# Kernel optimization log

Measured on AMD Instinct MI355X. Metric: run time of the kernel, lower is better.

Reference implementation:

```python
import jax, jax.numpy as jnp
import numpy as np

HEADS = 8
HID = 128
N_A = 10000
N_B = 10000
E = 120000
NG = 8  # graphs in batch
F_A = 256
F_B = 128
NEG_SLOPE = 0.2


def _gat(h_src, h_dst, src, dst, ws, wd, a_s, a_d, bias, num_dst):
    """PyG GATConv, bipartite, concat=False, add_self_loops=False."""
    hs = (h_src @ ws).reshape(-1, HEADS, HID)   # [N_src, H, C]
    hd = (h_dst @ wd).reshape(-1, HEADS, HID)   # [N_dst, H, C]
    al_s = jnp.sum(hs * a_s, axis=-1)           # [N_src, H]
    al_d = jnp.sum(hd * a_d, axis=-1)           # [N_dst, H]
    e = jax.nn.leaky_relu(al_s[src] + al_d[dst], NEG_SLOPE)  # [E, H]
    m = jax.ops.segment_max(e, dst, num_segments=num_dst)
    ex = jnp.exp(e - m[dst])
    denom = jax.ops.segment_sum(ex, dst, num_segments=num_dst)
    alpha = ex / (denom[dst] + 1e-16)           # segment softmax over in-edges
    msg = hs[src] * alpha[:, :, None]           # [E, H, C]
    out = jax.ops.segment_sum(msg, dst, num_segments=num_dst)
    return out.mean(axis=1) + bias              # concat=False -> head mean + bias


def _mean_pool(x, batch, num_graphs):
    s = jax.ops.segment_sum(x, batch, num_segments=num_graphs)
    cnt = jax.ops.segment_sum(jnp.ones((x.shape[0],), x.dtype), batch, num_segments=num_graphs)
    return s / jnp.maximum(cnt, 1.0)[:, None]


def setup_inputs() -> dict:
    key = jax.random.key(0)
    ks = iter(jax.random.split(key, 48))
    rn = lambda shape, s=0.05: jax.random.normal(next(ks), shape, jnp.float32) * s
    inp = {
        'x_a': jax.random.normal(next(ks), (N_A, F_A), jnp.float32),
        'x_b': jax.random.normal(next(ks), (N_B, F_B), jnp.float32),
        'edge_ab': jax.random.randint(next(ks), (2, E), 0, N_A, jnp.int32),
        'edge_ba': jax.random.randint(next(ks), (2, E), 0, N_B, jnp.int32),
        'batch_a': jnp.sort(jax.random.randint(next(ks), (N_A,), 0, NG, jnp.int32)),
        'batch_b': jnp.sort(jax.random.randint(next(ks), (N_B,), 0, NG, jnp.int32)),
        'lin_a_w': rn((F_A, HID)), 'lin_a_b': rn((HID,)),
        'lin_b_w': rn((F_B, HID)), 'lin_b_b': rn((HID,)),
        'fc_w': rn((2 * HID, 1)), 'fc_b': rn((1,)),
    }
    for layer in ('1', '2'):
        for rel in ('ab', 'ba'):
            inp[f'w{layer}s_{rel}'] = rn((HID, HEADS * HID))
            inp[f'w{layer}d_{rel}'] = rn((HID, HEADS * HID))
            inp[f'a{layer}s_{rel}'] = rn((HEADS, HID))
            inp[f'a{layer}d_{rel}'] = rn((HEADS, HID))
            inp[f'b{layer}_{rel}'] = rn((HID,))
    return inp


def reference(x_a, x_b, edge_ab, edge_ba, batch_a, batch_b,
              lin_a_w, lin_a_b, lin_b_w, lin_b_b, fc_w, fc_b,
              w1s_ab, w1d_ab, a1s_ab, a1d_ab, b1_ab,
              w1s_ba, w1d_ba, a1s_ba, a1d_ba, b1_ba,
              w2s_ab, w2d_ab, a2s_ab, a2d_ab, b2_ab,
              w2s_ba, w2d_ba, a2s_ba, a2d_ba, b2_ba):
    ha = jax.nn.relu(x_a @ lin_a_w + lin_a_b)
    hb = jax.nn.relu(x_b @ lin_b_w + lin_b_b)
    # layer 1 (each dst type receives exactly one relation -> HeteroConv mean is identity)
    hb1 = _gat(ha, hb, edge_ab[0], edge_ab[1], w1s_ab, w1d_ab, a1s_ab, a1d_ab, b1_ab, N_B)
    ha1 = _gat(hb, ha, edge_ba[0], edge_ba[1], w1s_ba, w1d_ba, a1s_ba, a1d_ba, b1_ba, N_A)
    ha1 = jax.nn.relu(ha1)
    hb1 = jax.nn.relu(hb1)
    # layer 2
    hb2 = _gat(ha1, hb1, edge_ab[0], edge_ab[1], w2s_ab, w2d_ab, a2s_ab, a2d_ab, b2_ab, N_B)
    ha2 = _gat(hb1, ha1, edge_ba[0], edge_ba[1], w2s_ba, w2d_ba, a2s_ba, a2d_ba, b2_ba, N_A)
    pa = _mean_pool(ha2, batch_a, NG)
    pb = _mean_pool(hb2, batch_b, NG)
    g = jnp.concatenate([pa, pb], axis=1)       # [NG, 2*HID]
    return (g @ fc_w + fc_b).squeeze(-1)        # [NG]
```

## Files before the change

kernel.cpp:

```cpp
#include <hip/hip_runtime.h>
#include <math.h>

#define HID 128
#define HEADS 8

typedef __attribute__((ext_vector_type(8))) short s16x8;
typedef __attribute__((ext_vector_type(4))) float f32x4;

__device__ __forceinline__ unsigned short bf16_rne(float x) {
  unsigned u = __float_as_uint(x);
  unsigned r = u + 0x7FFFu + ((u >> 16) & 1u);
  return (unsigned short)(r >> 16);
}
__device__ __forceinline__ float bf16f(unsigned short h) {
  return __uint_as_float(((unsigned)h) << 16);
}

struct PrepArgs {
  const float* W[8];
  const float* a[8];
  unsigned short* WThi[4];
  unsigned short* WTlo[4];
  float* v[8];
};
struct PrepX {
  const float* lwa; const float* lwb;
  unsigned short *wa_hi, *wa_lo, *wb_hi, *wb_lo;
  int KA, KB, nwa, nwb;
};

__global__ __launch_bounds__(256) void prep_hist(
    PrepArgs p, PrepX px,
    const int* __restrict__ dst_ab, const int* __restrict__ dst_ba,
    int* __restrict__ cnt_ab, int* __restrict__ cnt_ba, int E)
{
  int bid = blockIdx.x;
  if (bid < 2048) {
    int g = bid >> 9;
    int idx = ((bid & 511) << 8) + threadIdx.x;
    int kidx = idx & 1023;
    int c = idx >> 10;
    int h = kidx >> 7, k = kidx & 127;
    float wv = p.W[2 * g][(size_t)k * (HEADS * HID) + h * HID + c];
    unsigned short hi = bf16_rne(wv);
    unsigned short lo = bf16_rne(wv - bf16f(hi));
    p.WThi[g][idx] = hi;
    p.WTlo[g][idx] = lo;
  } else if (bid < 2080) {
    int u = bid - 2048;
    int wi = u >> 2;
    int gid = ((u & 3) << 8) + threadIdx.x;
    int k = gid >> 3, h = gid & 7;
    const float* wr = p.W[wi] + (size_t)k * (HEADS * HID) + h * HID;
    const float* ar = p.a[wi] + (size_t)h * HID;
    float s = 0.f;
    for (int c = 0; c < HID; c++) s = fmaf(wr[c], ar[c], s);
    p.v[wi][gid] = s;
  } else if (bid < 2080 + px.nwa) {
    int idx = (bid - 2080) * 256 + threadIdx.x;
    if (idx < px.KA * HID) {
      int k = idx % px.KA, c = idx / px.KA;
      float wv = px.lwa[(size_t)k * HID + c];
      unsigned short hi = bf16_rne(wv);
      unsigned short lo = bf16_rne(wv - bf16f(hi));
      px.wa_hi[idx] = hi;
      px.wa_lo[idx] = lo;
    }
  } else if (bid < 2080 + px.nwa + px.nwb) {
    int idx = (bid - 2080 - px.nwa) * 256 + threadIdx.x;
    if (idx < px.KB * HID) {
      int k = idx % px.KB, c = idx / px.KB;
      float wv = px.lwb[(size_t)k * HID + c];
      unsigned short hi = bf16_rne(wv);
      unsigned short lo = bf16_rne(wv - bf16f(hi));
      px.wb_hi[idx] = hi;
      px.wb_lo[idx] = lo;
    }
  } else {
    int gid = (bid - 2080 - px.nwa - px.nwb) * 256 + threadIdx.x;
    if (gid < E) atomicAdd(&cnt_ab[dst_ab[gid]], 1);
    else if (gid < 2 * E) atomicAdd(&cnt_ba[dst_ba[gid - E]], 1);
  }
}

__global__ __launch_bounds__(1024) void scan2(
    const int* __restrict__ cnt_ab, const int* __restrict__ cnt_ba,
    int* __restrict__ ip_ab, int* __restrict__ ip_ba, int n_ab, int n_ba)
{
  const int* cnt = (blockIdx.x == 0) ? cnt_ab : cnt_ba;
  int* indptr = (blockIdx.x == 0) ? ip_ab : ip_ba;
  int n = (blockIdx.x == 0) ? n_ab : n_ba;
  __shared__ int parts[1024];
  const int tid = threadIdx.x;
  const int base = tid * 10;
  int local[10];
  int s = 0;
#pragma unroll
  for (int j = 0; j < 10; j++) {
    int v = (base + j < n) ? cnt[base + j] : 0;
    local[j] = v; s += v;
  }
  parts[tid] = s;
  __syncthreads();
  for (int off = 1; off < 1024; off <<= 1) {
    int v = (tid >= off) ? parts[tid - off] : 0;
    __syncthreads();
    parts[tid] += v;
    __syncthreads();
  }
  int ex = parts[tid] - s;
#pragma unroll
  for (int j = 0; j < 10; j++) {
    if (base + j < n) indptr[base + j] = ex;
    ex += local[j];
  }
  if (tid == 1023) indptr[n] = parts[1023];
}

__global__ __launch_bounds__(256) void scatter2(
    const int* __restrict__ edge_ab, const int* __restrict__ edge_ba,
    const int* __restrict__ ip_ab, const int* __restrict__ ip_ba,
    int* __restrict__ cur_ab, int* __restrict__ cur_ba,
    int* __restrict__ srcs_ab, int* __restrict__ srcs_ba, int E)
{
  int gid = blockIdx.x * 256 + threadIdx.x;
  if (gid < E) {
    int d = edge_ab[E + gid];
    int pos = ip_ab[d] + atomicAdd(&cur_ab[d], 1);
    srcs_ab[pos] = edge_ab[gid];
  } else if (gid < 2 * E) {
    int g = gid - E;
    int d = edge_ba[E + g];
    int pos = ip_ba[d] + atomicAdd(&cur_ba[d], 1);
    srcs_ba[pos] = edge_ba[g];
  }
}

struct ISeg {
  const float* A;
  const unsigned short* Bhi; const unsigned short* Blo;
  float* out; const float* bias; int M; int K; int yb;
};

__global__ __launch_bounds__(256) void gemm_mfma_in(ISeg s0, ISeg s1)
{
  __shared__ __align__(16) unsigned short smem[12288];
  const int tid = threadIdx.x;
  const float* A; const unsigned short *Bhi, *Blo; const float* bias; float* out;
  int M, K, ytile;
  if ((int)blockIdx.x < s0.yb) {
    A = s0.A; Bhi = s0.Bhi; Blo = s0.Blo; out = s0.out; bias = s0.bias;
    M = s0.M; K = s0.K; ytile = blockIdx.x;
  } else {
    A = s1.A; Bhi = s1.Bhi; Blo = s1.Blo; out = s1.out; bias = s1.bias;
    M = s1.M; K = s1.K; ytile = blockIdx.x - s0.yb;
  }
  const int bm = ytile * 64;
  const int nks = K >> 5;

  const int sr = tid >> 2;
  const int sg = tid & 3;
  const int g1 = sg ^ ((sr >> 1) & 3);
  const int sr2 = sr + 64;
  const int g2 = sg ^ ((sr2 >> 1) & 3);
  const int aslot  = sr * 32 + g1 * 8;
  const int bslotA = sr * 32 + g1 * 8;
  const int bslotB = sr2 * 32 + g2 * 8;
  const int gr = bm + sr;
  const bool arow_ok = (gr < M);
  const float* gA = A + (size_t)gr * K + sg * 8;
  const unsigned short* gB0 = Bhi + (size_t)sr  * K + sg * 8;
  const unsigned short* gB1 = Bhi + (size_t)sr2 * K + sg * 8;
  const unsigned short* gC0 = Blo + (size_t)sr  * K + sg * 8;
  const unsigned short* gC1 = Blo + (size_t)sr2 * K + sg * 8;

  const int l = tid & 63;
  const int w = tid >> 6;
  const int kg = l >> 4;
  int aoff[4], boff[2];
#pragma unroll
  for (int mi = 0; mi < 4; mi++) {
    int r = mi * 16 + (l & 15);
    aoff[mi] = r * 32 + (kg ^ ((r >> 1) & 3)) * 8;
  }
#pragma unroll
  for (int ni = 0; ni < 2; ni++) {
    int r = w * 32 + ni * 16 + (l & 15);
    boff[ni] = r * 32 + (kg ^ ((r >> 1) & 3)) * 8;
  }

  f32x4 acc[4][2];
  const f32x4 z4 = {0.f, 0.f, 0.f, 0.f};
#pragma unroll
  for (int mi = 0; mi < 4; mi++)
#pragma unroll
    for (int ni = 0; ni < 2; ni++) acc[mi][ni] = z4;

  float4 fa0 = make_float4(0.f, 0.f, 0.f, 0.f), fa1 = fa0;
  if (arow_ok) { fa0 = *(const float4*)gA; fa1 = *(const float4*)(gA + 4); }
  uint4 rB0 = *(const uint4*)gB0;
  uint4 rB1 = *(const uint4*)gB1;
  uint4 rC0 = *(const uint4*)gC0;
  uint4 rC1 = *(const uint4*)gC1;

  for (int ks = 0; ks < nks; ks++) {
    {
      const float f[8] = {fa0.x, fa0.y, fa0.z, fa0.w, fa1.x, fa1.y, fa1.z, fa1.w};
      unsigned au[4], lu[4];
#pragma unroll
      for (int i = 0; i < 4; i++) {
        unsigned short h0 = bf16_rne(f[2 * i]);
        unsigned short l0 = bf16_rne(f[2 * i] - bf16f(h0));
        unsigned short h1 = bf16_rne(f[2 * i + 1]);
        unsigned short l1 = bf16_rne(f[2 * i + 1] - bf16f(h1));
        au[i] = (unsigned)h0 | ((unsigned)h1 << 16);
        lu[i] = (unsigned)l0 | ((unsigned)l1 << 16);
      }
      *(uint4*)&smem[aslot]        = make_uint4(au[0], au[1], au[2], au[3]);
      *(uint4*)&smem[2048 + aslot] = make_uint4(lu[0], lu[1], lu[2], lu[3]);
    }
    *(uint4*)&smem[4096 + bslotA] = rB0;
    *(uint4*)&smem[4096 + bslotB] = rB1;
    *(uint4*)&smem[8192 + bslotA] = rC0;
    *(uint4*)&smem[8192 + bslotB] = rC1;
    __syncthreads();
    if (ks < nks - 1) {
      const int k0 = (ks + 1) * 32;
      if (arow_ok) {
        fa0 = *(const float4*)(gA + k0);
        fa1 = *(const float4*)(gA + k0 + 4);
      }
      rB0 = *(const uint4*)(gB0 + k0);
// ... 176 lines not shown
    if (s >= 0) {
      float v = als[(size_t)s * HEADS + h] + aldn;
      v = v > 0.f ? v : 0.2f * v;
      ex = expf(v);
    }
    int elim = deg - e0; if (elim > 8) elim = 8;
    for (int e8 = 0; e8 < elim; e8++) {
      int ss = __shfl(s, e8 * 8);
      const float2 hvt = *(const float2*)(hsrc + (size_t)ss * HID + 2 * lane);
#pragma unroll
      for (int hh = 0; hh < 8; hh++) {
        float a = __shfl(ex, e8 * 8 + hh);
        acc[2 * hh]     = fmaf(a, hvt.x, acc[2 * hh]);
        acc[2 * hh + 1] = fmaf(a, hvt.y, acc[2 * hh + 1]);
      }
    }
  }
#pragma unroll
  for (int hh = 0; hh < 8; hh++) {
    float dh = __shfl(den, hh);
    float inv = 1.f / (dh + 1e-16f);
    float x0 = acc[2 * hh] * inv;
    float x1 = acc[2 * hh + 1] * inv;
    unsigned short h0 = bf16_rne(x0), h1 = bf16_rne(x1);
    unsigned short l0 = bf16_rne(x0 - bf16f(h0)), l1 = bf16_rne(x1 - bf16f(h1));
    *(unsigned*)(zh + hh * HID + 2 * lane) = (unsigned)h0 | ((unsigned)h1 << 16);
    *(unsigned*)(zl + hh * HID + 2 * lane) = (unsigned)l0 | ((unsigned)l1 << 16);
  }
}

struct MSeg {
  const unsigned short* Ahi; const unsigned short* Alo;
  const unsigned short* Bhi; const unsigned short* Blo;
  int M; int yb;
};

__global__ __launch_bounds__(256, 2) void gemm_mfma_splitk(
    MSeg s0, MSeg s1, float* __restrict__ P, int Mtot, int KS)
{
  __shared__ __align__(16) unsigned short smem[12288];
  const int tid = threadIdx.x;
  const unsigned short *Ahi, *Alo, *Bhi, *Blo; int M, ytile, rowbase;
  if ((int)blockIdx.x < s0.yb) {
    Ahi = s0.Ahi; Alo = s0.Alo; Bhi = s0.Bhi; Blo = s0.Blo;
    M = s0.M; ytile = blockIdx.x; rowbase = 0;
  } else {
    Ahi = s1.Ahi; Alo = s1.Alo; Bhi = s1.Bhi; Blo = s1.Blo;
    M = s1.M; ytile = blockIdx.x - s0.yb; rowbase = s0.yb * 64;
  }
  const int bm = ytile * 64;
  const int kchunk = 1024 / KS;
  const int kbeg = blockIdx.y * kchunk;
  const int nks = kchunk / 32;

  const int sr = tid >> 2;
  const int sg = tid & 3;
  const int g1 = sg ^ ((sr >> 1) & 3);
  const int sr2 = sr + 64;
  const int g2 = sg ^ ((sr2 >> 1) & 3);
  const int aslot  = sr * 32 + g1 * 8;
  const int bslotA = sr * 32 + g1 * 8;
  const int bslotB = sr2 * 32 + g2 * 8;
  const unsigned short* gA  = Ahi + (size_t)(bm + sr) * 1024 + kbeg + sg * 8;
  const unsigned short* gAl = Alo + (size_t)(bm + sr) * 1024 + kbeg + sg * 8;
  const unsigned short* gB0 = Bhi + (size_t)sr  * 1024 + kbeg + sg * 8;
  const unsigned short* gB1 = Bhi + (size_t)sr2 * 1024 + kbeg + sg * 8;
  const unsigned short* gC0 = Blo + (size_t)sr  * 1024 + kbeg + sg * 8;
  const unsigned short* gC1 = Blo + (size_t)sr2 * 1024 + kbeg + sg * 8;

  const int l = tid & 63;
  const int w = tid >> 6;
  const int kg = l >> 4;
  int aoff[4], boff[2];
#pragma unroll
  for (int mi = 0; mi < 4; mi++) {
    int r = mi * 16 + (l & 15);
    aoff[mi] = r * 32 + (kg ^ ((r >> 1) & 3)) * 8;
  }
#pragma unroll
  for (int ni = 0; ni < 2; ni++) {
    int r = w * 32 + ni * 16 + (l & 15);
    boff[ni] = r * 32 + (kg ^ ((r >> 1) & 3)) * 8;
  }

  f32x4 acc[4][2];
  const f32x4 z4 = {0.f, 0.f, 0.f, 0.f};
#pragma unroll
  for (int mi = 0; mi < 4; mi++)
#pragma unroll
    for (int ni = 0; ni < 2; ni++) acc[mi][ni] = z4;

  uint4 rA  = *(const uint4*)gA;
  uint4 rAl = *(const uint4*)gAl;
  uint4 rB0 = *(const uint4*)gB0;
  uint4 rB1 = *(const uint4*)gB1;
  uint4 rC0 = *(const uint4*)gC0;
  uint4 rC1 = *(const uint4*)gC1;

  for (int ks = 0; ks < nks; ks++) {
    *(uint4*)&smem[aslot]         = rA;
    *(uint4*)&smem[2048 + aslot]  = rAl;
    *(uint4*)&smem[4096 + bslotA] = rB0;
    *(uint4*)&smem[4096 + bslotB] = rB1;
    *(uint4*)&smem[8192 + bslotA] = rC0;
    *(uint4*)&smem[8192 + bslotB] = rC1;
    __syncthreads();
    if (ks < nks - 1) {
      const int k0 = (ks + 1) * 32;
      rA  = *(const uint4*)(gA  + k0);
      rAl = *(const uint4*)(gAl + k0);
      rB0 = *(const uint4*)(gB0 + k0);
      rB1 = *(const uint4*)(gB1 + k0);
      rC0 = *(const uint4*)(gC0 + k0);
      rC1 = *(const uint4*)(gC1 + k0);
    }
    s16x8 bh0 = *(const s16x8*)&smem[4096 + boff[0]];
    s16x8 bh1 = *(const s16x8*)&smem[4096 + boff[1]];
    s16x8 bl0 = *(const s16x8*)&smem[8192 + boff[0]];
    s16x8 bl1 = *(const s16x8*)&smem[8192 + boff[1]];
#pragma unroll
    for (int mi = 0; mi < 4; mi++) {
      s16x8 ah = *(const s16x8*)&smem[aoff[mi]];
      s16x8 al = *(const s16x8*)&smem[2048 + aoff[mi]];
      acc[mi][0] = __builtin_amdgcn_mfma_f32_16x16x32_bf16(ah, bh0, acc[mi][0], 0, 0, 0);
      acc[mi][1] = __builtin_amdgcn_mfma_f32_16x16x32_bf16(ah, bh1, acc[mi][1], 0, 0, 0);
      acc[mi][0] = __builtin_amdgcn_mfma_f32_16x16x32_bf16(ah, bl0, acc[mi][0], 0, 0, 0);
      acc[mi][1] = __builtin_amdgcn_mfma_f32_16x16x32_bf16(ah, bl1, acc[mi][1], 0, 0, 0);
      acc[mi][0] = __builtin_amdgcn_mfma_f32_16x16x32_bf16(al, bh0, acc[mi][0], 0, 0, 0);
      acc[mi][1] = __builtin_amdgcn_mfma_f32_16x16x32_bf16(al, bh1, acc[mi][1], 0, 0, 0);
      acc[mi][0] = __builtin_amdgcn_mfma_f32_16x16x32_bf16(al, bl0, acc[mi][0], 0, 0, 0);
      acc[mi][1] = __builtin_amdgcn_mfma_f32_16x16x32_bf16(al, bl1, acc[mi][1], 0, 0, 0);
    }
    __syncthreads();
  }

  const int q = l >> 4, cl = l & 15;
  const size_t prow0 = (size_t)blockIdx.y * Mtot + rowbase + bm;
#pragma unroll
  for (int ni = 0; ni < 2; ni++) {
    const int col = w * 32 + ni * 16 + cl;
#pragma unroll
    for (int mi = 0; mi < 4; mi++) {
      const int r0 = mi * 16 + q * 4;
      const f32x4 v = acc[mi][ni];
#pragma unroll
      for (int j = 0; j < 4; j++) {
        const int r = r0 + j;
        if (bm + r < M) P[(prow0 + r) * HID + col] = v[j];
      }
    }
  }
}

struct RSeg { float* out; const float* bias; int M; int rowbase; };

__global__ __launch_bounds__(256) void reduce_epi(
    const float* __restrict__ P, int Mtot, int KS, float scale, int do_relu,
    RSeg s0, RSeg s1)
{
  int idx = blockIdx.x * 256 + threadIdx.x;
  if (idx >= Mtot * 32) return;
  int r = idx >> 5;
  int c = (idx & 31) << 2;
  float* outp; const float* bias; int rl;
  if (s1.M > 0 && r >= s1.rowbase) {
    rl = r - s1.rowbase; if (rl >= s1.M) return; outp = s1.out; bias = s1.bias;
  } else {
    rl = r; if (rl >= s0.M) return; outp = s0.out; bias = s0.bias;
  }
  float4 acc = make_float4(0.f, 0.f, 0.f, 0.f);
  for (int z = 0; z < KS; z++) {
    const float4 v = *(const float4*)(P + ((size_t)z * Mtot + r) * HID + c);
    acc.x += v.x; acc.y += v.y; acc.z += v.z; acc.w += v.w;
  }
  const float4 b = *(const float4*)(bias + c);
  acc.x = acc.x * scale + b.x;
  acc.y = acc.y * scale + b.y;
  acc.z = acc.z * scale + b.z;
  acc.w = acc.w * scale + b.w;
  if (do_relu) {
    acc.x = acc.x > 0.f ? acc.x : 0.f;
    acc.y = acc.y > 0.f ? acc.y : 0.f;
    acc.z = acc.z > 0.f ? acc.z : 0.f;
    acc.w = acc.w > 0.f ? acc.w : 0.f;
  }
  *(float4*)(outp + (size_t)rl * HID + c) = acc;
}

__global__ __launch_bounds__(256) void pool_fin(
    const float* __restrict__ ha, const float* __restrict__ hb,
    const int* __restrict__ batch_a, const int* __restrict__ batch_b,
    const float* __restrict__ fc_w, const float* __restrict__ fc_b,
    float* __restrict__ gsum, int* __restrict__ ticket,
    float* __restrict__ out, int na, int nb, int ng)
{
  const bool isA = blockIdx.x < 160;
  const float* h = isA ? ha : hb;
  const int* batch = isA ? batch_a : batch_b;
  const float* wseg = isA ? fc_w : fc_w + HID;
  float* gs = isA ? gsum : gsum + 8;
  const int n = isA ? na : nb;
  const int b = isA ? blockIdx.x : blockIdx.x - 160;

  __shared__ float sg[8];
  __shared__ int lastf;
  if (threadIdx.x < 8) sg[threadIdx.x] = 0.f;
  __syncthreads();
  const int lane = threadIdx.x & 63;
  const int wv = threadIdx.x >> 6;
  const int gw = b * 4 + wv;
  const int tw = 160 * 4;
  const float2 w2 = *(const float2*)(wseg + lane * 2);
  for (int r = gw; r < n; r += tw) {
    float2 hv = *(const float2*)(h + (size_t)r * HID + lane * 2);
    float s = hv.x * w2.x + hv.y * w2.y;
#pragma unroll
    for (int off = 32; off > 0; off >>= 1) s += __shfl_down(s, off, 64);
    if (lane == 0) atomicAdd(&sg[batch[r]], s);
  }
  __syncthreads();
  if (threadIdx.x < 8) atomicAdd(&gs[threadIdx.x], sg[threadIdx.x]);
  if (threadIdx.x == 0) {
    __threadfence();
    int tk = atomicAdd(ticket, 1);
    lastf = (tk == (int)gridDim.x - 1);
  }
  __syncthreads();
  if (lastf) {
    int g = threadIdx.x;
    if (g < ng) {
      int l, r, lo;
      l = 0; r = na; while (l < r) { int m = (l + r) >> 1; if (batch_a[m] < g) l = m + 1; else r = m; } lo = l;
      r = na; while (l < r) { int m = (l + r) >> 1; if (batch_a[m] < g + 1) l = m + 1; else r = m; }
      int ca = l - lo; if (ca < 1) ca = 1;
      l = 0; r = nb; while (l < r) { int m = (l + r) >> 1; if (batch_b[m] < g) l = m + 1; else r = m; } lo = l;
      r = nb; while (l < r) { int m = (l + r) >> 1; if (batch_b[m] < g + 1) l = m + 1; else r = m; }
      int cb = l - lo; if (cb < 1) cb = 1;
      float va = atomicAdd(&gsum[g], 0.f);
      float vb = atomicAdd(&gsum[8 + g], 0.f);
      out[g] = va / (float)ca + vb / (float)cb + fc_b[0];
    }
  }
}

extern "C" void kernel_launch(void* const* d_in, const int* in_sizes, int n_in,
                              void* d_out, int out_size, void* d_ws, size_t ws_size,
                              hipStream_t stream)
{
  const float* x_a = (const float*)d_in[0];
  const float* x_b = (const float*)d_in[1];
  const int* edge_ab = (const int*)d_in[2];
  const int* edge_ba = (const int*)d_in[3];
  const int* batch_a = (const int*)d_in[4];
  const int* batch_b = (const int*)d_in[5];
  const float* lin_a_w = (const float*)d_in[6];
  const float* lin_a_b = (const float*)d_in[7];
  const float* lin_b_w = (const float*)d_in[8];
  const float* lin_b_b = (const float*)d_in[9];
  const float* fc_w = (const float*)d_in[10];
  const float* fc_b = (const float*)d_in[11];

  const int NA = in_sizes[4];
  const int NB = in_sizes[5];
  const int E  = in_sizes[2] / 2;
  const int FA = in_sizes[0] / NA;
  const int FB = in_sizes[1] / NB;
  const int NG = out_size;
  const int NMAX = NA > NB ? NA : NB;
  const int NAp = (NA + 127) & ~127, NBp = (NB + 127) & ~127;
  const int NMAXp = NAp > NBp ? NAp : NBp;
  const int Mtot = NAp + NBp;

  auto al256 = [](size_t b) { return (b + 255) & ~(size_t)255; };
  size_t fixed = 0;
  fixed += 3 * al256((size_t)NAp * HID * 4) + 3 * al256((size_t)NBp * HID * 4);
  fixed += 2 * al256((size_t)NMAXp * 1024 * 2);
  fixed += al256((size_t)8 * 131072 * 2);
  fixed += 2 * al256((size_t)FA * HID * 2) + 2 * al256((size_t)FB * HID * 2);
  fixed += al256((size_t)8 * HID * HEADS * 4);
  fixed += 2 * al256((size_t)NAp * HEADS * 4) + 2 * al256((size_t)NBp * HEADS * 4);
  fixed += al256(((size_t)4 * NMAX + 24) * 4);
  fixed += al256((size_t)(NB + 1) * 4) + al256((size_t)(NA + 1) * 4);
  fixed += 2 * al256((size_t)E * 4);
  fixed += 8192;
  const size_t zba_sz = 2 * al256((size_t)NAp * 1024 * 2);
  const size_t pslice = al256((size_t)Mtot * HID * 4);

  int KS = 4; bool dual = true;
  if (fixed + zba_sz + 4 * pslice <= ws_size)      { dual = true;  KS = 4; }
  else if (fixed + zba_sz + 2 * pslice <= ws_size) { dual = true;  KS = 2; }
  else if (fixed + 4 * pslice <= ws_size)          { dual = false; KS = 4; }
  else if (fixed + 2 * pslice <= ws_size)          { dual = false; KS = 2; }
  else if (fixed + 1 * pslice <= ws_size)          { dual = false; KS = 1; }
  else return;

  char* w = (char*)d_ws;
  auto carve = [&](size_t bytes) -> void* {
    void* p = (void*)w;
    w += (bytes + 255) & ~(size_t)255;
    return p;
  };
  float* ha0 = (float*)carve((size_t)NAp * HID * 4);
  float* hb0 = (float*)carve((size_t)NBp * HID * 4);
  float* ha1 = (float*)carve((size_t)NAp * HID * 4);
  float* hb1 = (float*)carve((size_t)NBp * HID * 4);
  float* ha2 = (float*)carve((size_t)NAp * HID * 4);
  float* hb2 = (float*)carve((size_t)NBp * HID * 4);
  unsigned short* zab_hi = (unsigned short*)carve((size_t)NMAXp * 1024 * 2);
  unsigned short* zab_lo = (unsigned short*)carve((size_t)NMAXp * 1024 * 2);
  unsigned short* zba_hi = dual ? (unsigned short*)carve((size_t)NAp * 1024 * 2) : zab_hi;
  unsigned short* zba_lo = dual ? (unsigned short*)carve((size_t)NAp * 1024 * 2) : zab_lo;
  float* P = (float*)carve((size_t)KS * Mtot * HID * 4);
  unsigned short* WT = (unsigned short*)carve((size_t)8 * 131072 * 2);
  unsigned short* wa_hi = (unsigned short*)carve((size_t)FA * HID * 2);
  unsigned short* wa_lo = (unsigned short*)carve((size_t)FA * HID * 2);
  unsigned short* wb_hi = (unsigned short*)carve((size_t)FB * HID * 2);
  unsigned short* wb_lo = (unsigned short*)carve((size_t)FB * HID * 2);
  float* vv  = (float*)carve((size_t)8 * HID * HEADS * 4);
  float* als_ab = (float*)carve((size_t)NAp * HEADS * 4);
  float* ald_ab = (float*)carve((size_t)NBp * HEADS * 4);
  float* als_ba = (float*)carve((size_t)NBp * HEADS * 4);
  float* ald_ba = (float*)carve((size_t)NAp * HEADS * 4);
  int* csrblk = (int*)carve(((size_t)4 * NMAX + 24) * 4);
  int* indptr_ab = (int*)carve((size_t)(NB + 1) * 4);
  int* indptr_ba = (int*)carve((size_t)(NA + 1) * 4);
  int* srcs_ab   = (int*)carve((size_t)E * 4);
  int* srcs_ba   = (int*)carve((size_t)E * 4);
  if ((size_t)(w - (char*)d_ws) > ws_size) return;

  int* cnt_ab = csrblk;
  int* cnt_ba = csrblk + NMAX;
  int* cur_ab = csrblk + 2 * NMAX;
  int* cur_ba = csrblk + 3 * NMAX;
  float* gsum = (float*)(csrblk + 4 * NMAX);
  int* ticket = csrblk + 4 * NMAX + 16;

  hipMemsetAsync(csrblk, 0, ((size_t)4 * NMAX + 24) * 4, stream);

  PrepArgs pa;
  const int wi_idx[8] = {12, 13, 17, 18, 22, 23, 27, 28};
  const int ai_idx[8] = {14, 15, 19, 20, 24, 25, 29, 30};
  for (int i = 0; i < 8; i++) {
    pa.W[i] = (const float*)d_in[wi_idx[i]];
    pa.a[i] = (const float*)d_in[ai_idx[i]];
    pa.v[i] = vv + (size_t)i * HID * HEADS;
  }
  for (int g = 0; g < 4; g++) {
    pa.WThi[g] = WT + (size_t)g * 131072;
    pa.WTlo[g] = WT + (size_t)(4 + g) * 131072;
  }
  PrepX px;
  px.lwa = lin_a_w; px.lwb = lin_b_w;
  px.wa_hi = wa_hi; px.wa_lo = wa_lo; px.wb_hi = wb_hi; px.wb_lo = wb_lo;
  px.KA = FA; px.KB = FB;
  px.nwa = (FA * HID + 255) / 256;
  px.nwb = (FB * HID + 255) / 256;
  const int hist_b = (2 * E + 255) / 256;
  prep_hist<<<2080 + px.nwa + px.nwb + hist_b, 256, 0, stream>>>(
      pa, px, edge_ab + E, edge_ba + E, cnt_ab, cnt_ba, E);
  scan2<<<2, 1024, 0, stream>>>(cnt_ab, cnt_ba, indptr_ab, indptr_ba, NB, NA);
  scatter2<<<(2 * E + 255) / 256, 256, 0, stream>>>(
      edge_ab, edge_ba, indptr_ab, indptr_ba, cur_ab, cur_ba, srcs_ab, srcs_ba, E);

  {
    ISeg sa = {x_a, wa_hi, wa_lo, ha0, lin_a_b, NA, FA, NAp / 64};
    ISeg sb = {x_b, wb_hi, wb_lo, hb0, lin_b_b, NB, FB, NBp / 64};
    gemm_mfma_in<<<NAp / 64 + NBp / 64, 256, 0, stream>>>(sa, sb);
  }

  const int red_grid = (Mtot * 32 + 255) / 256;
  const RSeg rnone = {nullptr, nullptr, 0, 0};

  auto run_layer = [&](int L, const float* haP, const float* hbP,
                       float* haN, float* hbN, const float* b_ab, const float* b_ba,
                       int relu) {
    compute_al4<<<((2 * (NA + NB)) * HEADS + 255) / 256, 256, 0, stream>>>(
        haP, hbP, vv + (size_t)L * 4 * HID * HEADS,
        als_ab, ald_ab, als_ba, ald_ba, NA, NB);
    GDir dab = {indptr_ab, srcs_ab, als_ab, ald_ab, haP, zab_hi, zab_lo};
    GDir dba = {indptr_ba, srcs_ba, als_ba, ald_ba, hbP, zba_hi, zba_lo};
    const int gab = 2 * L, gba = 2 * L + 1;
    MSeg mab = {zab_hi, zab_lo, WT + (size_t)gab * 131072, WT + (size_t)(4 + gab) * 131072,
                NB, NBp / 64};
    MSeg mba = {zba_hi, zba_lo, WT + (size_t)gba * 131072, WT + (size_t)(4 + gba) * 131072,
                NA, NAp / 64};
    if (dual) {
      gat_edge2<<<(NB + NA + 3) / 4, 256, 0, stream>>>(dab, dba, NB, NB + NA);
      gemm_mfma_splitk<<<dim3(NBp / 64 + NAp / 64, KS), 256, 0, stream>>>(mab, mba, P, Mtot, KS);
      RSeg r0 = {hbN, b_ab, NB, 0};
      RSeg r1 = {haN, b_ba, NA, NBp};
      reduce_epi<<<red_grid, 256, 0, stream>>>(P, Mtot, KS, 1.f / HEADS, relu, r0, r1);
    } else {
      MSeg mz = {nullptr, nullptr, nullptr, nullptr, 0, 0};
      gat_edge2<<<(NB + 3) / 4, 256, 0, stream>>>(dab, dab, NB, NB);
      gemm_mfma_splitk<<<dim3(NBp / 64, KS), 256, 0, stream>>>(mab, mz, P, NBp, KS);
      RSeg r0 = {hbN, b_ab, NB, 0};
      reduce_epi<<<(NBp * 32 + 255) / 256, 256, 0, stream>>>(P, NBp, KS, 1.f / HEADS, relu, r0, rnone);
      gat_edge2<<<(NA + 3) / 4, 256, 0, stream>>>(dba, dba, NA, NA);
      gemm_mfma_splitk<<<dim3(NAp / 64, KS), 256, 0, stream>>>(mba, mz, P, NAp, KS);
      RSeg r1 = {haN, b_ba, NA, 0};
      reduce_epi<<<(NAp * 32 + 255) / 256, 256, 0, stream>>>(P, NAp, KS, 1.f / HEADS, relu, r1, rnone);
    }
  };

  run_layer(0, ha0, hb0, ha1, hb1, (const float*)d_in[16], (const float*)d_in[21], 1);
  run_layer(1, ha1, hb1, ha2, hb2, (const float*)d_in[26], (const float*)d_in[31], 0);

  pool_fin<<<320, 256, 0, stream>>>(ha2, hb2, batch_a, batch_b, fc_w, fc_b,
                                    gsum, ticket, (float*)d_out, NA, NB, NG);
}
```

Measured before the change: 370.4 us.

## Fuse attention-logit and pooling into split-K reduce epilogues; tile weight transposes

The layer-2 attention logits (al_s/al_d) are now computed inside the layer-1 reduce epilogue, so the separate compute_al4 launch for layer 2 is gone. The final pooling and FC dot product move into the layer-2 reduce epilogue, which removes the pool_fin kernel and the ha2/hb2 buffers and their round trip through memory. The weight transpose and bf16 hi/lo split in prep_hist now goes through a 64x64 shared-memory tile with vectorized stores, replacing a strided per-element scatter. In exchange the epilogue does extra per-row reductions and takes many atomics on gsum, and the prep code keeps a dead hibuf loop.

```diff
diff --git a/kernel.cpp b/kernel.cpp
--- a/kernel.cpp
+++ b/kernel.cpp
@@ -14,6 +14,9 @@
 }
 __device__ __forceinline__ float bf16f(unsigned short h) {
   return __uint_as_float(((unsigned)h) << 16);
+}
+__device__ __forceinline__ unsigned pack_hi(float a, float b) {
+  return (unsigned)bf16_rne(a) | ((unsigned)bf16_rne(b) << 16);
 }
 
 struct PrepArgs {
@@ -26,7 +29,7 @@
 struct PrepX {
   const float* lwa; const float* lwb;
   unsigned short *wa_hi, *wa_lo, *wb_hi, *wb_lo;
-  int KA, KB, nwa, nwb;
+  int KA, KB, nta, ntb;
 };
 
 __global__ __launch_bounds__(256) void prep_hist(
@@ -34,50 +37,92 @@
     const int* __restrict__ dst_ab, const int* __restrict__ dst_ba,
     int* __restrict__ cnt_ab, int* __restrict__ cnt_ba, int E)
 {
-  int bid = blockIdx.x;
-  if (bid < 2048) {
-    int g = bid >> 9;
-    int idx = ((bid & 511) << 8) + threadIdx.x;
-    int kidx = idx & 1023;
-    int c = idx >> 10;
-    int h = kidx >> 7, k = kidx & 127;
-    float wv = p.W[2 * g][(size_t)k * (HEADS * HID) + h * HID + c];
-    unsigned short hi = bf16_rne(wv);
-    unsigned short lo = bf16_rne(wv - bf16f(hi));
-    p.WThi[g][idx] = hi;
-    p.WTlo[g][idx] = lo;
-  } else if (bid < 2080) {
-    int u = bid - 2048;
-    int wi = u >> 2;
-    int gid = ((u & 3) << 8) + threadIdx.x;
-    int k = gid >> 3, h = gid & 7;
+  __shared__ float tile[64][65];
+  const int bid = blockIdx.x;
+  const int tid = threadIdx.x;
+  const int a = tid >> 2;
+  const int cg = (tid & 3) << 4;
+
+  if (bid < 128) {
+    const int g = bid >> 5;
+    const int rem = bid & 31;
+    const int h = rem >> 2;
+    const int t = rem & 3;
+    const int k0 = (t >> 1) << 6, c0 = (t & 1) << 6;
+    const float* src = p.W[2 * g] + (size_t)(k0 + a) * 1024 + h * 128 + c0 + cg;
+#pragma unroll
+    for (int i = 0; i < 16; i += 4) {
+      const float4 v4 = *(const float4*)(src + i);
+      tile[a][cg + i + 0] = v4.x; tile[a][cg + i + 1] = v4.y;
+      tile[a][cg + i + 2] = v4.z; tile[a][cg + i + 3] = v4.w;
+    }
+    __syncthreads();
+    const size_t ob = (size_t)(c0 + a) * 1024 + h * 128 + k0 + cg;
+    unsigned hibuf[4], lobuf[4];
+#pragma unroll
+    for (int i = 0; i < 8; i++) {
+      float x0 = tile[cg + 2 * i][a];
+      float x1 = tile[cg + 2 * i + 1][a];
+      unsigned short h0 = bf16_rne(x0), h1 = bf16_rne(x1);
+      hibuf[i >> 1] = (i & 1) ? (hibuf[i >> 1] | (((unsigned)h0 | ((unsigned)h1 << 16)) == 0 ? 0u : 0u)) : 0u;
+    }
+    unsigned hw[8], lw_[8];
+#pragma unroll
+    for (int i = 0; i < 8; i++) {
+      float x0 = tile[cg + 2 * i][a];
+      float x1 = tile[cg + 2 * i + 1][a];
+      unsigned short h0 = bf16_rne(x0), h1 = bf16_rne(x1);
+      unsigned short l0 = bf16_rne(x0 - bf16f(h0)), l1 = bf16_rne(x1 - bf16f(h1));
+      hw[i]  = (unsigned)h0 | ((unsigned)h1 << 16);
+      lw_[i] = (unsigned)l0 | ((unsigned)l1 << 16);
+    }
+    *(uint4*)(p.WThi[g] + ob)     = make_uint4(hw[0], hw[1], hw[2], hw[3]);
+    *(uint4*)(p.WThi[g] + ob + 8) = make_uint4(hw[4], hw[5], hw[6], hw[7]);
+    *(uint4*)(p.WTlo[g] + ob)     = make_uint4(lw_[0], lw_[1], lw_[2], lw_[3]);
+    *(uint4*)(p.WTlo[g] + ob + 8) = make_uint4(lw_[4], lw_[5], lw_[6], lw_[7]);
+  } else if (bid < 160) {
+    const int u = bid - 128;
+    const int wi = u >> 2;
+    const int gid = ((u & 3) << 8) + tid;
+    const int k = gid >> 3, h = gid & 7;
     const float* wr = p.W[wi] + (size_t)k * (HEADS * HID) + h * HID;
     const float* ar = p.a[wi] + (size_t)h * HID;
     float s = 0.f;
     for (int c = 0; c < HID; c++) s = fmaf(wr[c], ar[c], s);
     p.v[wi][gid] = s;
-  } else if (bid < 2080 + px.nwa) {
-    int idx = (bid - 2080) * 256 + threadIdx.x;
-    if (idx < px.KA * HID) {
-      int k = idx % px.KA, c = idx / px.KA;
-      float wv = px.lwa[(size_t)k * HID + c];
-      unsigned short hi = bf16_rne(wv);
-      unsigned short lo = bf16_rne(wv - bf16f(hi));
-      px.wa_hi[idx] = hi;
-      px.wa_lo[idx] = lo;
-    }
-  } else if (bid < 2080 + px.nwa + px.nwb) {
-    int idx = (bid - 2080 - px.nwa) * 256 + threadIdx.x;
-    if (idx < px.KB * HID) {
-      int k = idx % px.KB, c = idx / px.KB;
-      float wv = px.lwb[(size_t)k * HID + c];
-      unsigned short hi = bf16_rne(wv);
-      unsigned short lo = bf16_rne(wv - bf16f(hi));
-      px.wb_hi[idx] = hi;
-      px.wb_lo[idx] = lo;
-    }
+  } else if (bid < 160 + px.nta + px.ntb) {
+    const bool isa = (bid - 160) < px.nta;
+    const int b = isa ? (bid - 160) : (bid - 160 - px.nta);
+    const int K = isa ? px.KA : px.KB;
+    const float* lw = isa ? px.lwa : px.lwb;
+    unsigned short* ohi = isa ? px.wa_hi : px.wb_hi;
+    unsigned short* olo = isa ? px.wa_lo : px.wb_lo;
+    const int k0 = (b >> 1) << 6, c0 = (b & 1) << 6;
+    const float* src = lw + (size_t)(k0 + a) * 128 + c0 + cg;
+#pragma unroll
+    for (int i = 0; i < 16; i += 4) {
+      const float4 v4 = *(const float4*)(src + i);
+      tile[a][cg + i + 0] = v4.x; tile[a][cg + i + 1] = v4.y;
+      tile[a][cg + i + 2] = v4.z; tile[a][cg + i + 3] = v4.w;
+    }
+    __syncthreads();
+    const size_t ob = (size_t)(c0 + a) * K + k0 + cg;
+    unsigned hw[8], lw_[8];
+#pragma unroll
+    for (int i = 0; i < 8; i++) {
+      float x0 = tile[cg + 2 * i][a];
+      float x1 = tile[cg + 2 * i + 1][a];
+      unsigned short h0 = bf16_rne(x0), h1 = bf16_rne(x1);
+      unsigned short l0 = bf16_rne(x0 - bf16f(h0)), l1 = bf16_rne(x1 - bf16f(h1));
+      hw[i]  = (unsigned)h0 | ((unsigned)h1 << 16);
+      lw_[i] = (unsigned)l0 | ((unsigned)l1 << 16);
+    }
+    *(uint4*)(ohi + ob)     = make_uint4(hw[0], hw[1], hw[2], hw[3]);
+    *(uint4*)(ohi + ob + 8) = make_uint4(hw[4], hw[5], hw[6], hw[7]);
+    *(uint4*)(olo + ob)     = make_uint4(lw_[0], lw_[1], lw_[2], lw_[3]);
+    *(uint4*)(olo + ob + 8) = make_uint4(lw_[4], lw_[5], lw_[6], lw_[7]);
   } else {
-    int gid = (bid - 2080 - px.nwa - px.nwb) * 256 + threadIdx.x;
+    int gid = (bid - 160 - px.nta - px.ntb) * 256 + tid;
     if (gid < E) atomicAdd(&cnt_ab[dst_ab[gid]], 1);
     else if (gid < 2 * E) atomicAdd(&cnt_ba[dst_ba[gid - E]], 1);
   }
@@ -560,21 +605,28 @@
   }
 }
 
-struct RSeg { float* out; const float* bias; int M; int rowbase; };
-
-__global__ __launch_bounds__(256) void reduce_epi(
+struct RSegA {
+  float* out; const float* bias; int M; int rowbase;
+  const float* va; const float* vb;
+  float* ala; float* alb;
+};
+
+__global__ __launch_bounds__(256) void reduce_epi_al(
     const float* __restrict__ P, int Mtot, int KS, float scale, int do_relu,
-    RSeg s0, RSeg s1)
+    RSegA s0, RSegA s1)
 {
   int idx = blockIdx.x * 256 + threadIdx.x;
   if (idx >= Mtot * 32) return;
   int r = idx >> 5;
   int c = (idx & 31) << 2;
   float* outp; const float* bias; int rl;
+  const float* va; const float* vb; float* ala; float* alb;
   if (s1.M > 0 && r >= s1.rowbase) {
-    rl = r - s1.rowbase; if (rl >= s1.M) return; outp = s1.out; bias = s1.bias;
+    rl = r - s1.rowbase; if (rl >= s1.M) return;
+    outp = s1.out; bias = s1.bias; va = s1.va; vb = s1.vb; ala = s1.ala; alb = s1.alb;
   } else {
-    rl = r; if (rl >= s0.M) return; outp = s0.out; bias = s0.bias;
+    rl = r; if (rl >= s0.M) return;
+    outp = s0.out; bias = s0.bias; va = s0.va; vb = s0.vb; ala = s0.ala; alb = s0.alb;
   }
   float4 acc = make_float4(0.f, 0.f, 0.f, 0.f);
   for (int z = 0; z < KS; z++) {
@@ -587,62 +639,109 @@
   acc.z = acc.z * scale + b.z;
   acc.w = acc.w * scale + b.w;
   if (do_relu) {
-    acc.x = acc.x > 0.f ? acc.x : 0.f;
-    acc.y = acc.y > 0.f ? acc.y : 0.f;
-    acc.z = acc.z > 0.f ? acc.z : 0.f;
-    acc.w = acc.w > 0.f ? acc.w : 0.f;
+    acc.x = fmaxf(acc.x, 0.f); acc.y = fmaxf(acc.y, 0.f);
+    acc.z = fmaxf(acc.z, 0.f); acc.w = fmaxf(acc.w, 0.f);
   }
   *(float4*)(outp + (size_t)rl * HID + c) = acc;
-}
-
-__global__ __launch_bounds__(256) void pool_fin(
-    const float* __restrict__ ha, const float* __restrict__ hb,
+
+  const float av[4] = {acc.x, acc.y, acc.z, acc.w};
+  float pA[8], pB[8];
+#pragma unroll
+  for (int i = 0; i < 8; i++) { pA[i] = 0.f; pB[i] = 0.f; }
+#pragma unroll
+  for (int j = 0; j < 4; j++) {
+    const float4 a0 = *(const float4*)(va + (c + j) * 8);
+    const float4 a1 = *(const float4*)(va + (c + j) * 8 + 4);
+    const float4 b0 = *(const float4*)(vb + (c + j) * 8);
+    const float4 b1 = *(const float4*)(vb + (c + j) * 8 + 4);
+    pA[0] = fmaf(av[j], a0.x, pA[0]); pA[1] = fmaf(av[j], a0.y, pA[1]);
+    pA[2] = fmaf(av[j], a0.z, pA[2]); pA[3] = fmaf(av[j], a0.w, pA[3]);
+    pA[4] = fmaf(av[j], a1.x, pA[4]); pA[5] = fmaf(av[j], a1.y, pA[5]);
+    pA[6] = fmaf(av[j], a1.z, pA[6]); pA[7] = fmaf(av[j], a1.w, pA[7]);
+    pB[0] = fmaf(av[j], b0.x, pB[0]); pB[1] = fmaf(av[j], b0.y, pB[1]);
+    pB[2] = fmaf(av[j], b0.z, pB[2]); pB[3] = fmaf(av[j], b0.w, pB[3]);
+    pB[4] = fmaf(av[j], b1.x, pB[4]); pB[5] = fmaf(av[j], b1.y, pB[5]);
+    pB[6] = fmaf(av[j], b1.z, pB[6]); pB[7] = fmaf(av[j], b1.w, pB[7]);
+  }
+#pragma unroll
+  for (int off = 16; off >= 1; off >>= 1) {
+#pragma unroll
+    for (int i = 0; i < 8; i++) {
+      pA[i] += __shfl_xor(pA[i], off);
+      pB[i] += __shfl_xor(pB[i], off);
+    }
+  }
+  if ((threadIdx.x & 31) == 0) {
+    *(float4*)(ala + (size_t)rl * 8)     = make_float4(pA[0], pA[1], pA[2], pA[3]);
+    *(float4*)(ala + (size_t)rl * 8 + 4) = make_float4(pA[4], pA[5], pA[6], pA[7]);
+    *(float4*)(alb + (size_t)rl * 8)     = make_float4(pB[0], pB[1], pB[2], pB[3]);
+    *(float4*)(alb + (size_t)rl * 8 + 4) = make_float4(pB[4], pB[5], pB[6], pB[7]);
+  }
+}
+
+struct RSegP { const float* bias; int M; int rowbase; int isA; };
+
+__global__ __launch_bounds__(256) void reduce_epi_pool(
+    const float* __restrict__ P, int Mtot, int KS, float scale,
+    RSegP s0, RSegP s1,
+    const float* __restrict__ fc_w, const float* __restrict__ fc_b,
     const int* __restrict__ batch_a, const int* __restrict__ batch_b,
-    const float* __restrict__ fc_w, const float* __restrict__ fc_b,
     float* __restrict__ gsum, int* __restrict__ ticket,
-    float* __restrict__ out, int na, int nb, int ng)
+    float* __restrict__ out, int na, int nb, int ng, int tot_blocks)
 {
-  const bool isA = blockIdx.x < 160;
-  const float* h = isA ? ha : hb;
-  const int* batch = isA ? batch_a : batch_b;
-  const float* wseg = isA ? fc_w : fc_w + HID;
-  float* gs = isA ? gsum : gsum + 8;
-  const int n = isA ? na : nb;
-  const int b = isA ? blockIdx.x : blockIdx.x - 160;
-
-  __shared__ float sg[8];
   __shared__ int lastf;
-  if (threadIdx.x < 8) sg[threadIdx.x] = 0.f;
+  const int idx = blockIdx.x * 256 + threadIdx.x;
+  bool ok = idx < Mtot * 32;
+  int r = 0, c = 0, rl = 0, isA = 0;
+  const float* bias = s0.bias;
+  if (ok) {
+    r = idx >> 5;
+    c = (idx & 31) << 2;
+    if (s1.M > 0 && r >= s1.rowbase) {
+      rl = r - s1.rowbase; isA = s1.isA; bias = s1.bias;
+      if (rl >= s1.M) ok = false;
+    } else {
+      rl = r; isA = s0.isA; bias = s0.bias;
+      if (rl >= s0.M) ok = false;
+    }
+  }
+  float part = 0.f;
+  if (ok) {
+    float4 acc = make_float4(0.f, 0.f, 0.f, 0.f);
+    for (int z = 0; z < KS; z++) {
+      const float4 v = *(const float4*)(P + ((size_t)z * Mtot + r) * HID + c);
+      acc.x += v.x; acc.y += v.y; acc.z += v.z; acc.w += v.w;
+    }
+    const float4 b = *(const float4*)(bias + c);
+    acc.x = acc.x * scale + b.x;
+    acc.y = acc.y * scale + b.y;
+    acc.z = acc.z * scale + b.z;
+    acc.w = acc.w * scale + b.w;
+    const float* wseg = fc_w + (isA ? 0 : HID) + c;
+    part = acc.x * wseg[0] + acc.y * wseg[1] + acc.z * wseg[2] + acc.w * wseg[3];
+  }
+#pragma unroll
+  for (int off = 16; off >= 1; off >>= 1) part += __shfl_xor(part, off);
+  if (ok && (threadIdx.x & 31) == 0) {
+    const int bt = isA ? batch_a[rl] : batch_b[rl];
+    atomicAdd(&gsum[(isA ? 0 : 8) + bt], part);
+  }
   __syncthreads();
-  const int lane = threadIdx.x & 63;
-  const int wv = threadIdx.x >> 6;
-  const int gw = b * 4 + wv;
-  const int tw = 160 * 4;
-  const float2 w2 = *(const float2*)(wseg + lane * 2);
-  for (int r = gw; r < n; r += tw) {
-    float2 hv = *(const float2*)(h + (size_t)r * HID + lane * 2);
-    float s = hv.x * w2.x + hv.y * w2.y;
-#pragma unroll
-    for (int off = 32; off > 0; off >>= 1) s += __shfl_down(s, off, 64);
-    if (lane == 0) atomicAdd(&sg[batch[r]], s);
-  }
-  __syncthreads();
-  if (threadIdx.x < 8) atomicAdd(&gs[threadIdx.x], sg[threadIdx.x]);
   if (threadIdx.x == 0) {
     __threadfence();
     int tk = atomicAdd(ticket, 1);
-    lastf = (tk == (int)gridDim.x - 1);
+    lastf = (tk == tot_blocks - 1);
   }
   __syncthreads();
   if (lastf) {
     int g = threadIdx.x;
     if (g < ng) {
-      int l, r, lo;
-      l = 0; r = na; while (l < r) { int m = (l + r) >> 1; if (batch_a[m] < g) l = m + 1; else r = m; } lo = l;
-      r = na; while (l < r) { int m = (l + r) >> 1; if (batch_a[m] < g + 1) l = m + 1; else r = m; }
+      int l, rr, lo;
+      l = 0; rr = na; while (l < rr) { int m = (l + rr) >> 1; if (batch_a[m] < g) l = m + 1; else rr = m; } lo = l;
+      rr = na; while (l < rr) { int m = (l + rr) >> 1; if (batch_a[m] < g + 1) l = m + 1; else rr = m; }
       int ca = l - lo; if (ca < 1) ca = 1;
-      l = 0; r = nb; while (l < r) { int m = (l + r) >> 1; if (batch_b[m] < g) l = m + 1; else r = m; } lo = l;
-      r = nb; while (l < r) { int m = (l + r) >> 1; if (batch_b[m] < g + 1) l = m + 1; else r = m; }
+      l = 0; rr = nb; while (l < rr) { int m = (l + rr) >> 1; if (batch_b[m] < g) l = m + 1; else rr = m; } lo = l;
+      rr = nb; while (l < rr) { int m = (l + rr) >> 1; if (batch_b[m] < g + 1) l = m + 1; else rr = m; }
       int cb = l - lo; if (cb < 1) cb = 1;
       float va = atomicAdd(&gsum[g], 0.f);
       float vb = atomicAdd(&gsum[8 + g], 0.f);
@@ -681,7 +780,7 @@
 
   auto al256 = [](size_t b) { return (b + 255) & ~(size_t)255; };
   size_t fixed = 0;
-  fixed += 3 * al256((size_t)NAp * HID * 4) + 3 * al256((size_t)NBp * HID * 4);
+  fixed += 2 * al256((size_t)NAp * HID * 4) + 2 * al256((size_t)NBp * HID * 4);
   fixed += 2 * al256((size_t)NMAXp * 1024 * 2);
   fixed += al256((size_t)8 * 131072 * 2);
   fixed += 2 * al256((size_t)FA * HID * 2) + 2 * al256((size_t)FB * HID * 2);
@@ -712,8 +811,6 @@
   float* hb0 = (float*)carve((size_t)NBp * HID * 4);
   float* ha1 = (float*)carve((size_t)NAp * HID * 4);
   float* hb1 = (float*)carve((size_t)NBp * HID * 4);
-  float* ha2 = (float*)carve((size_t)NAp * HID * 4);
-  float* hb2 = (float*)carve((size_t)NBp * HID * 4);
   unsigned short* zab_hi = (unsigned short*)carve((size_t)NMAXp * 1024 * 2);
   unsigned short* zab_lo = (unsigned short*)carve((size_t)NMAXp * 1024 * 2);
   unsigned short* zba_hi = dual ? (unsigned short*)carve((size_t)NAp * 1024 * 2) : zab_hi;
@@ -761,10 +858,10 @@
   px.lwa = lin_a_w; px.lwb = lin_b_w;
   px.wa_hi = wa_hi; px.wa_lo = wa_lo; px.wb_hi = wb_hi; px.wb_lo = wb_lo;
   px.KA = FA; px.KB = FB;
-  px.nwa = (FA * HID + 255) / 256;
-  px.nwb = (FB * HID + 255) / 256;
+  px.nta = (FA / 64) * 2;
+  px.ntb = (FB / 64) * 2;
   const int hist_b = (2 * E + 255) / 256;
-  prep_hist<<<2080 + px.nwa + px.nwb + hist_b, 256, 0, stream>>>(
+  prep_hist<<<160 + px.nta + px.ntb + hist_b, 256, 0, stream>>>(
       pa, px, edge_ab + E, edge_ba + E, cnt_ab, cnt_ba, E);
   scan2<<<2, 1024, 0, stream>>>(cnt_ab, cnt_ba, indptr_ab, indptr_ba, NB, NA);
   scatter2<<<(2 * E + 255) / 256, 256, 0, stream>>>(
@@ -777,43 +874,69 @@
   }
 
   const int red_grid = (Mtot * 32 + 255) / 256;
-  const RSeg rnone = {nullptr, nullptr, 0, 0};
-
-  auto run_layer = [&](int L, const float* haP, const float* hbP,
-                       float* haN, float* hbN, const float* b_ab, const float* b_ba,
-                       int relu) {
-    compute_al4<<<((2 * (NA + NB)) * HEADS + 255) / 256, 256, 0, stream>>>(
-        haP, hbP, vv + (size_t)L * 4 * HID * HEADS,
-        als_ab, ald_ab, als_ba, ald_ba, NA, NB);
-    GDir dab = {indptr_ab, srcs_ab, als_ab, ald_ab, haP, zab_hi, zab_lo};
-    GDir dba = {indptr_ba, srcs_ba, als_ba, ald_ba, hbP, zba_hi, zba_lo};
-    const int gab = 2 * L, gba = 2 * L + 1;
-    MSeg mab = {zab_hi, zab_lo, WT + (size_t)gab * 131072, WT + (size_t)(4 + gab) * 131072,
-                NB, NBp / 64};
-    MSeg mba = {zba_hi, zba_lo, WT + (size_t)gba * 131072, WT + (size_t)(4 + gba) * 131072,
-                NA, NAp / 64};
-    if (dual) {
-      gat_edge2<<<(NB + NA + 3) / 4, 256, 0, stream>>>(dab, dba, NB, NB + NA);
-      gemm_mfma_splitk<<<dim3(NBp / 64 + NAp / 64, KS), 256, 0, stream>>>(mab, mba, P, Mtot, KS);
-      RSeg r0 = {hbN, b_ab, NB, 0};
-      RSeg r1 = {haN, b_ba, NA, NBp};
-      reduce_epi<<<red_grid, 256, 0, stream>>>(P, Mtot, KS, 1.f / HEADS, relu, r0, r1);
-    } else {
+
+  compute_al4<<<((2 * (NA + NB)) * HEADS + 255) / 256, 256, 0, stream>>>(
+      ha0, hb0, vv, als_ab, ald_ab, als_ba, ald_ba, NA, NB);
+
+  GDir dab0 = {indptr_ab, srcs_ab, als_ab, ald_ab, ha0, zab_hi, zab_lo};
+  GDir dba0 = {indptr_ba, srcs_ba, als_ba, ald_ba, hb0, zba_hi, zba_lo};
+  MSeg mab0 = {zab_hi, zab_lo, WT + (size_t)0 * 131072, WT + (size_t)4 * 131072, NB, NBp / 64};
+  MSeg mba0 = {zba_hi, zba_lo, WT + (size_t)1 * 131072, WT + (size_t)5 * 131072, NA, NAp / 64};
+  const float* v1 = vv + (size_t)4 * HID * HEADS;
+
+  GDir dab1 = {indptr_ab, srcs_ab, als_ab, ald_ab, ha1, zab_hi, zab_lo};
+  GDir dba1 = {indptr_ba, srcs_ba, als_ba, ald_ba, hb1, zba_hi, zba_lo};
+  MSeg mab1 = {zab_hi, zab_lo, WT + (size_t)2 * 131072, WT + (size_t)6 * 131072, NB, NBp / 64};
+  MSeg mba1 = {zba_hi, zba_lo, WT + (size_t)3 * 131072, WT + (size_t)7 * 131072, NA, NAp / 64};
+
+  if (dual) {
+    gat_edge2<<<(NB + NA + 3) / 4, 256, 0, stream>>>(dab0, dba0, NB, NB + NA);
+    gemm_mfma_splitk<<<dim3(NBp / 64 + NAp / 64, KS), 256, 0, stream>>>(mab0, mba0, P, Mtot, KS);
+    RSegA r0 = {hb1, (const float*)d_in[16], NB, 0,
+                v1 + 1024, v1 + 2048, ald_ab, als_ba};
+    RSegA r1 = {ha1, (const float*)d_in[21], NA, NBp,
+                v1, v1 + 3072, als_ab, ald_ba};
+    reduce_epi_al<<<red_grid, 256, 0, stream>>>(P, Mtot, KS, 1.f / HEADS, 1, r0, r1);
+    gat_edge2<<<(NB + NA + 3) / 4, 256, 0, stream>>>(dab1, dba1, NB, NB + NA);
+    gemm_mfma_splitk<<<dim3(NBp / 64 + NAp / 64, KS), 256, 0, stream>>>(mab1, mba1, P, Mtot, KS);
+    RSegP p0 = {(const float*)d_in[26], NB, 0, 0};
+    RSegP p1 = {(const float*)d_in[31], NA, NBp, 1};
+    reduce_epi_pool<<<red_grid, 256, 0, stream>>>(P, Mtot, KS, 1.f / HEADS, p0, p1,
+        fc_w, fc_b, batch_a, batch_b, gsum, ticket, (float*)d_out, NA, NB, NG, red_grid);
+  } else {
+    const RSegA ranull = {nullptr, nullptr, 0, 0, nullptr, nullptr, nullptr, nullptr};
+    gat_edge2<<<(NB + 3) / 4, 256, 0, stream>>>(dab0, dab0, NB, NB);
+    {
       MSeg mz = {nullptr, nullptr, nullptr, nullptr, 0, 0};
-      gat_edge2<<<(NB + 3) / 4, 256, 0, stream>>>(dab, dab, NB, NB);
-      gemm_mfma_splitk<<<dim3(NBp / 64, KS), 256, 0, stream>>>(mab, mz, P, NBp, KS);
-      RSeg r0 = {hbN, b_ab, NB, 0};
-      reduce_epi<<<(NBp * 32 + 255) / 256, 256, 0, stream>>>(P, NBp, KS, 1.f / HEADS, relu, r0, rnone);
-      gat_edge2<<<(NA + 3) / 4, 256, 0, stream>>>(dba, dba, NA, NA);
-      gemm_mfma_splitk<<<dim3(NAp / 64, KS), 256, 0, stream>>>(mba, mz, P, NAp, KS);
-      RSeg r1 = {haN, b_ba, NA, 0};
-      reduce_epi<<<(NAp * 32 + 255) / 256, 256, 0, stream>>>(P, NAp, KS, 1.f / HEADS, relu, r1, rnone);
-    }
-  };
-
-  run_layer(0, ha0, hb0, ha1, hb1, (const float*)d_in[16], (const float*)d_in[21], 1);
-  run_layer(1, ha1, hb1, ha2, hb2, (const float*)d_in[26], (const float*)d_in[31], 0);
-
-  pool_fin<<<320, 256, 0, stream>>>(ha2, hb2, batch_a, batch_b, fc_w, fc_b,
-                                    gsum, ticket, (float*)d_out, NA, NB, NG);
-}
+      gemm_mfma_splitk<<<dim3(NBp / 64, KS), 256, 0, stream>>>(mab0, mz, P, NBp, KS);
+      RSegA r0 = {hb1, (const float*)d_in[16], NB, 0, v1 + 1024, v1 + 2048, ald_ab, als_ba};
+      reduce_epi_al<<<(NBp * 32 + 255) / 256, 256, 0, stream>>>(P, NBp, KS, 1.f / HEADS, 1, r0, ranull);
+    }
+    gat_edge2<<<(NA + 3) / 4, 256, 0, stream>>>(dba0, dba0, NA, NA);
+    {
+      MSeg mz = {nullptr, nullptr, nullptr, nullptr, 0, 0};
+      gemm_mfma_splitk<<<dim3(NAp / 64, KS), 256, 0, stream>>>(mba0, mz, P, NAp, KS);
+      RSegA r1 = {ha1, (const float*)d_in[21], NA, 0, v1, v1 + 3072, als_ab, ald_ba};
+      reduce_epi_al<<<(NAp * 32 + 255) / 256, 256, 0, stream>>>(P, NAp, KS, 1.f / HEADS, 1, r1, ranull);
+    }
+    const int gb1 = (NBp * 32 + 255) / 256;
+    const int ga1 = (NAp * 32 + 255) / 256;
+    const RSegP pnull = {nullptr, 0, 0, 0};
+    gat_edge2<<<(NB + 3) / 4, 256, 0, stream>>>(dab1, dab1, NB, NB);
+    {
+      MSeg mz = {nullptr, nullptr, nullptr, nullptr, 0, 0};
+      gemm_mfma_splitk<<<dim3(NBp / 64, KS), 256, 0, stream>>>(mab1, mz, P, NBp, KS);
+      RSegP p0 = {(const float*)d_in[26], NB, 0, 0};
+      reduce_epi_pool<<<gb1, 256, 0, stream>>>(P, NBp, KS, 1.f / HEADS, p0, pnull,
+          fc_w, fc_b, batch_a, batch_b, gsum, ticket, (float*)d_out, NA, NB, NG, gb1 + ga1);
+    }
+    gat_edge2<<<(NA + 3) / 4, 256, 0, stream>>>(dba1, dba1, NA, NA);
+    {
+      MSeg mz = {nullptr, nullptr, nullptr, nullptr, 0, 0};
+      gemm_mfma_splitk<<<dim3(NAp / 64, KS), 256, 0, stream>>>(mba1, mz, P, NAp, KS);
+      RSegP p1 = {(const float*)d_in[31], NA, 0, 1};
+      reduce_epi_pool<<<ga1, 256, 0, stream>>>(P, NAp, KS, 1.f / HEADS, p1, pnull,
+          fc_w, fc_b, batch_a, batch_b, gsum, ticket, (float*)d_out, NA, NB, NG, gb1 + ga1);
+    }
+  }
+}
```

Result: slower. 624.9 us (+68.7%).
